# Performance work log

Hardware: AMD Instinct MI355X
Metric: run time of the kernel (lower is better)

Reference implementation:

```python
import jax, jax.numpy as jnp
import numpy as np

NUM_USERS = 100000
NUM_ITEMS = 50000
N = NUM_USERS + NUM_ITEMS
D = 64
NNZ = 4000000
BATCH = 8192
NUM_LAYERS = 3


def setup_inputs() -> dict:
    key = jax.random.key(0)
    k = jax.random.split(key, 8)
    return {
        "user_emb": jax.random.normal(k[0], (NUM_USERS, D), jnp.float32) * 0.1,
        "item_emb": jax.random.normal(k[1], (NUM_ITEMS, D), jnp.float32) * 0.1,
        # symmetric-normalized adjacency values (positive, ~1/degree scale)
        "adj_vals": jax.random.uniform(k[2], (NNZ,), jnp.float32) * (1.0 / 13.0),
        "adj_rows": jax.random.randint(k[3], (NNZ,), 0, N, jnp.int32),
        "adj_cols": jax.random.randint(k[4], (NNZ,), 0, N, jnp.int32),
        "user_idx": jax.random.randint(k[5], (BATCH,), 0, NUM_USERS, jnp.int32),
        "pos_idx": jax.random.randint(k[6], (BATCH,), 0, NUM_ITEMS, jnp.int32),
        "neg_idx": jax.random.randint(k[7], (BATCH,), 0, NUM_ITEMS, jnp.int32),
    }


def _propagate(user_emb, item_emb, adj_vals, adj_rows, adj_cols):
    # E0 = concat(user table, item table) along node axis -> [N, D]
    e = jnp.concatenate([user_emb, item_emb], axis=0)
    acc = e  # running sum over layer embeddings (E0 included)
    for _ in range(NUM_LAYERS):
        # SpMM: E <- A_norm @ E, via gather on cols + segment_sum on rows
        msg = adj_vals[:, None] * e[adj_cols]  # [NNZ, D]
        e = jax.ops.segment_sum(msg, adj_rows, num_segments=N)
        acc = acc + e
    final = acc / jnp.asarray(NUM_LAYERS + 1, e.dtype)  # mean-pool over layers
    return final


def reference(user_emb, item_emb, adj_vals, adj_rows, adj_cols,
              user_idx, pos_idx, neg_idx):
    final = _propagate(user_emb, item_emb, adj_vals, adj_rows, adj_cols)
    # split into user/item tables, then gather BPR triplets
    u = final[user_idx]                     # [B, D]
    p = final[NUM_USERS + pos_idx]          # [B, D]
    n = final[NUM_USERS + neg_idx]          # [B, D]
    pos_score = jnp.sum(u * p, axis=-1, keepdims=True)  # Dot(axes=1) -> [B,1]
    neg_score = jnp.sum(u * n, axis=-1, keepdims=True)
    return pos_score - neg_score
```

## Files before the change

### kernel.cpp

```cpp
#include <hip/hip_runtime.h>
#include <hip/hip_bf16.h>

#define D 64
#define MAXNB 1024
#define BIN_T 512
#define BIN_CHUNK 16384
#define BUCKET_BITS 9
#define BUCKET_SIZE 512
#define COL_MASK 0x3FFFF
#define ROW_SHIFT 18

static __device__ __forceinline__ float bf_lo(unsigned v) {
  return __uint_as_float(v << 16);
}
static __device__ __forceinline__ float bf_hi(unsigned v) {
  return __uint_as_float(v & 0xffff0000u);
}
static __device__ __forceinline__ unsigned pack_bf2(float a, float b) {
  __hip_bfloat16 x = __float2bfloat16(a);
  __hip_bfloat16 y = __float2bfloat16(b);
  unsigned short ux = *reinterpret_cast<unsigned short*>(&x);
  unsigned short uy = *reinterpret_cast<unsigned short*>(&y);
  return (unsigned)ux | ((unsigned)uy << 16);
}

__global__ __launch_bounds__(256) void convert_kernel(
    const float4* __restrict__ ue, const float4* __restrict__ ie,
    uint2* __restrict__ out, int nu4, int total4,
    int* __restrict__ counts, int nbp1) {
  int i = blockIdx.x * blockDim.x + threadIdx.x;
  if (i < nbp1) counts[i] = 0;
  if (i >= total4) return;
  float4 v = (i < nu4) ? ue[i] : ie[i - nu4];
  out[i] = make_uint2(pack_bf2(v.x, v.y), pack_bf2(v.z, v.w));
}

__global__ __launch_bounds__(256) void bucket_hist_kernel(
    const int* __restrict__ rows, int* __restrict__ counts, int nnz, int nb) {
  __shared__ int h[MAXNB];
  int t = threadIdx.x;
  for (int i = t; i < nb; i += 256) h[i] = 0;
  __syncthreads();
  for (int e = blockIdx.x * 256 + t; e < nnz; e += gridDim.x * 256)
    atomicAdd(&h[rows[e] >> BUCKET_BITS], 1);
  __syncthreads();
  for (int i = t; i < nb; i += 256)
    if (h[i]) atomicAdd(&counts[i], h[i]);
}

__global__ __launch_bounds__(1024) void bucket_scan_kernel(
    const int* __restrict__ counts, int* __restrict__ base,
    int* __restrict__ cursor, int nb) {
  __shared__ int lds[1024];
  int t = threadIdx.x;
  int v = (t < nb) ? counts[t] : 0;
  lds[t] = v;
  __syncthreads();
  for (int off = 1; off < 1024; off <<= 1) {
    int add = (t >= off) ? lds[t - off] : 0;
    __syncthreads();
    lds[t] += add;
    __syncthreads();
  }
  if (t < nb) {
    base[t + 1] = lds[t];
    cursor[t + 1] = lds[t];
  }
  if (t == 0) {
    base[0] = 0;
    cursor[0] = 0;
  }
}

__global__ __launch_bounds__(BIN_T) void bin_kernel(
    const float* __restrict__ vals, const int* __restrict__ rows,
    const int* __restrict__ cols, int* __restrict__ cursor,
    int2* __restrict__ binned, int nnz, int nb) {
  __shared__ int lh[MAXNB];
  int t = threadIdx.x;
  long long base_e = (long long)blockIdx.x * BIN_CHUNK;
  int end_e = (int)((base_e + BIN_CHUNK < (long long)nnz) ? base_e + BIN_CHUNK
                                                          : (long long)nnz);
  for (int i = t; i < nb; i += BIN_T) lh[i] = 0;
  __syncthreads();
  for (int e = (int)base_e + t; e < end_e; e += BIN_T)
    atomicAdd(&lh[rows[e] >> BUCKET_BITS], 1);
  __syncthreads();
  for (int i = t; i < nb; i += BIN_T) {
    int c = lh[i];
    if (c) lh[i] = atomicAdd(&cursor[i], c);
  }
  __syncthreads();
  for (int e = (int)base_e + t; e < end_e; e += BIN_T) {
    int r = rows[e];
    int pos = atomicAdd(&lh[r >> BUCKET_BITS], 1);
    binned[pos] = make_int2((cols[e] & COL_MASK) |
                                ((r & (BUCKET_SIZE - 1)) << ROW_SHIFT),
                            __float_as_int(vals[e]));
  }
}

__global__ __launch_bounds__(512) void place_kernel(
    const int2* __restrict__ binned, const int* __restrict__ base,
    int2* __restrict__ edges, int* __restrict__ row_start, int nrows, int nb) {
  __shared__ int rh[BUCKET_SIZE];
  __shared__ int cur[BUCKET_SIZE];
  int b = blockIdx.x;
  int t = threadIdx.x;
  int start = base[b];
  int end = base[b + 1];
  int r0 = b << BUCKET_BITS;
  rh[t] = 0;
  __syncthreads();
  for (int i = start + t; i < end; i += 512)
    atomicAdd(&rh[((unsigned)binned[i].x) >> ROW_SHIFT], 1);
  __syncthreads();
  int myc = rh[t];
  for (int off = 1; off < 512; off <<= 1) {
    int add = (t >= off) ? rh[t - off] : 0;
    __syncthreads();
    rh[t] += add;
    __syncthreads();
  }
  int excl = rh[t] - myc;
  int r = r0 + t;
  if (r < nrows) row_start[r] = start + excl;
  if (b == nb - 1 && t == 0) row_start[nrows] = end;
  cur[t] = start + excl;
  __syncthreads();
  for (int i = start + t; i < end; i += 512) {
    int2 rec = binned[i];
    unsigned x = (unsigned)rec.x;
    int pos = atomicAdd(&cur[x >> ROW_SHIFT], 1);
    edges[pos] = make_int2((int)(x & COL_MASK), rec.y);
  }
}

__global__ __launch_bounds__(256) void list_build_kernel(
    const int* __restrict__ ui, const int* __restrict__ pi,
    const int* __restrict__ ni, int* __restrict__ list, int batch, int nu) {
  int i = blockIdx.x * blockDim.x + threadIdx.x;
  if (i >= batch) return;
  list[3 * i] = ui[i];
  list[3 * i + 1] = nu + pi[i];
  list[3 * i + 2] = nu + ni[i];
}

__global__ __launch_bounds__(256) void spmm_bf16_kernel(
    const int* __restrict__ row_start, const int2* __restrict__ edges,
    const uint2* __restrict__ src,
    uint2* __restrict__ dst, int nrows) {
  int wid = (int)(((long long)blockIdx.x * blockDim.x + threadIdx.x) >> 6);
  if (wid >= nrows) return;
  int lane = threadIdx.x & 63;
  int sub = lane >> 4;
  int d4 = lane & 15;
  int s = row_start[wid];
  int e = row_start[wid + 1];
  float a0 = 0.f, a1 = 0.f, a2 = 0.f, a3 = 0.f;
  int j = s;
  for (; j + 16 <= e; j += 16) {
    int2 E[4];
    uint2 V[4];
    #pragma unroll
    for (int k = 0; k < 4; ++k) E[k] = edges[j + 4 * k + sub];
    #pragma unroll
    for (int k = 0; k < 4; ++k) V[k] = src[((long long)E[k].x << 4) + d4];
    #pragma unroll
    for (int k = 0; k < 4; ++k) {
      float w = __int_as_float(E[k].y);
      a0 = fmaf(w, bf_lo(V[k].x), a0);
      a1 = fmaf(w, bf_hi(V[k].x), a1);
      a2 = fmaf(w, bf_lo(V[k].y), a2);
      a3 = fmaf(w, bf_hi(V[k].y), a3);
    }
  }
  for (; j + 4 <= e; j += 4) {
    int2 ed = edges[j + sub];
    uint2 v = src[((long long)ed.x << 4) + d4];
    float w = __int_as_float(ed.y);
    a0 = fmaf(w, bf_lo(v.x), a0);
    a1 = fmaf(w, bf_hi(v.x), a1);
    a2 = fmaf(w, bf_lo(v.y), a2);
    a3 = fmaf(w, bf_hi(v.y), a3);
  }
  for (; j + 2 <= e; j += 2) {
    if ((lane & 31) < 16) {
      int2 ed = edges[j + (lane >> 5)];
      uint2 v = src[((long long)ed.x << 4) + d4];
      float w = __int_as_float(ed.y);
      a0 = fmaf(w, bf_lo(v.x), a0);
      a1 = fmaf(w, bf_hi(v.x), a1);
      a2 = fmaf(w, bf_lo(v.y), a2);
      a3 = fmaf(w, bf_hi(v.y), a3);
    }
  }
  if (j < e && sub == 0) {
    int2 ed = edges[j];
    uint2 v = src[((long long)ed.x << 4) + d4];
    float w = __int_as_float(ed.y);
    a0 = fmaf(w, bf_lo(v.x), a0);
    a1 = fmaf(w, bf_hi(v.x), a1);
    a2 = fmaf(w, bf_lo(v.y), a2);
    a3 = fmaf(w, bf_hi(v.y), a3);
  }
  a0 += __shfl_down(a0, 32, 64);
  a1 += __shfl_down(a1, 32, 64);
  a2 += __shfl_down(a2, 32, 64);
  a3 += __shfl_down(a3, 32, 64);
  a0 += __shfl_down(a0, 16, 64);
  a1 += __shfl_down(a1, 16, 64);
  a2 += __shfl_down(a2, 16, 64);
  a3 += __shfl_down(a3, 16, 64);
  if (lane < 16)
    dst[((long long)wid << 4) + d4] =
        make_uint2(pack_bf2(a0, a1), pack_bf2(a2, a3));
}

__global__ __launch_bounds__(256) void spmm_bf16_list_kernel(
    const int* __restrict__ row_start, const int2* __restrict__ edges,
    const uint2* __restrict__ src, uint2* __restrict__ dst,
    const int* __restrict__ list, int nlist) {
  int widx = (int)(((long long)blockIdx.x * blockDim.x + threadIdx.x) >> 6);
  if (widx >= nlist) return;
  int wid = list[widx];
  int lane = threadIdx.x & 63;
  int sub = lane >> 4;
  int d4 = lane & 15;
  int s = row_start[wid];
  int e = row_start[wid + 1];
  float a0 = 0.f, a1 = 0.f, a2 = 0.f, a3 = 0.f;
  int j = s;
  for (; j + 16 <= e; j += 16) {
    int2 E[4];
    uint2 V[4];
    #pragma unroll
    for (int k = 0; k < 4; ++k) E[k] = edges[j + 4 * k + sub];
    #pragma unroll
    for (int k = 0; k < 4; ++k) V[k] = src[((long long)E[k].x << 4) + d4];
    #pragma unroll
    for (int k = 0; k < 4; ++k) {
      float w = __int_as_float(E[k].y);
      a0 = fmaf(w, bf_lo(V[k].x), a0);
      a1 = fmaf(w, bf_hi(V[k].x), a1);
      a2 = fmaf(w, bf_lo(V[k].y), a2);
      a3 = fmaf(w, bf_hi(V[k].y), a3);
    }
  }
  for (; j + 4 <= e; j += 4) {
    int2 ed = edges[j + sub];
    uint2 v = src[((long long)ed.x << 4) + d4];
    float w = __int_as_float(ed.y);
    a0 = fmaf(w, bf_lo(v.x), a0);
    a1 = fmaf(w, bf_hi(v.x), a1);
    a2 = fmaf(w, bf_lo(v.y), a2);
    a3 = fmaf(w, bf_hi(v.y), a3);
  }
  for (; j + 2 <= e; j += 2) {
    if ((lane & 31) < 16) {
      int2 ed = edges[j + (lane >> 5)];
      uint2 v = src[((long long)ed.x << 4) + d4];
      float w = __int_as_float(ed.y);
      a0 = fmaf(w, bf_lo(v.x), a0);
      a1 = fmaf(w, bf_hi(v.x), a1);
      a2 = fmaf(w, bf_lo(v.y), a2);
      a3 = fmaf(w, bf_hi(v.y), a3);
    }
  }
  if (j < e && sub == 0) {
    int2 ed = edges[j];
    uint2 v = src[((long long)ed.x << 4) + d4];
    float w = __int_as_float(ed.y);
    a0 = fmaf(w, bf_lo(v.x), a0);
    a1 = fmaf(w, bf_hi(v.x), a1);
    a2 = fmaf(w, bf_lo(v.y), a2);
    a3 = fmaf(w, bf_hi(v.y), a3);
  }
  a0 += __shfl_down(a0, 32, 64);
  a1 += __shfl_down(a1, 32, 64);
  a2 += __shfl_down(a2, 32, 64);
  a3 += __shfl_down(a3, 32, 64);
  a0 += __shfl_down(a0, 16, 64);
  a1 += __shfl_down(a1, 16, 64);
  a2 += __shfl_down(a2, 16, 64);
  a3 += __shfl_down(a3, 16, 64);
  if (lane < 16)
    dst[((long long)wid << 4) + d4] =
        make_uint2(pack_bf2(a0, a1), pack_bf2(a2, a3));
}

__global__ __launch_bounds__(256) void score2_kernel(
    const float* __restrict__ ue, const float* __restrict__ ie,
    const unsigned* __restrict__ e1, const unsigned* __restrict__ e2,
    const unsigned* __restrict__ e3, const int* __restrict__ ui,
    const int* __restrict__ pi, const int* __restrict__ ni,
    float* __restrict__ out, int batch, int nu) {
  int w = (int)(((long long)blockIdx.x * blockDim.x + threadIdx.x) >> 6);
  int lane = threadIdx.x & 63;
  int half = lane >> 5;
  int d2 = lane & 31;
  int b = w * 2 + half;
  if (b >= batch) return;
  long long un = (long long)ui[b];
  int p = pi[b], n = ni[b];
  long long pn = (long long)(nu + p);
  long long nn_ = (long long)(nu + n);
  float2 U = *(const float2*)(ue + (un << 6) + (d2 << 1));
  float2 P = *(const float2*)(ie + ((long long)p << 6) + (d2 << 1));
  float2 Nv = *(const float2*)(ie + ((long long)n << 6) + (d2 << 1));
  unsigned v;
  v = e1[(un << 5) + d2]; U.x += bf_lo(v); U.y += bf_hi(v);
  v = e2[(un << 5) + d2]; U.x += bf_lo(v); U.y += bf_hi(v);
  v = e3[(un << 5) + d2]; U.x += bf_lo(v); U.y += bf_hi(v);
  v = e1[(pn << 5) + d2]; P.x += bf_lo(v); P.y += bf_hi(v);
  v = e2[(pn << 5) + d2]; P.x += bf_lo(v); P.y += bf_hi(v);
  v = e3[(pn << 5) + d2]; P.x += bf_lo(v); P.y += bf_hi(v);
  v = e1[(nn_ << 5) + d2]; Nv.x += bf_lo(v); Nv.y += bf_hi(v);
  v = e2[(nn_ << 5) + d2]; Nv.x += bf_lo(v); Nv.y += bf_hi(v);
  v = e3[(nn_ << 5) + d2]; Nv.x += bf_lo(v); Nv.y += bf_hi(v);
  float s = U.x * (P.x - Nv.x) + U.y * (P.y - Nv.y);
  #pragma unroll
  for (int off = 16; off; off >>= 1) s += __shfl_down(s, off, 32);
  if (d2 == 0) out[b] = s * (1.0f / 16.0f);
}

__global__ __launch_bounds__(256) void init_kernel(
    const float4* __restrict__ ue, const float4* __restrict__ ie,
    float4* __restrict__ e, float4* __restrict__ acc, int nu4, int total4) {
  int i = blockIdx.x * blockDim.x + threadIdx.x;
  if (i >= total4) return;
  float4 v = (i < nu4) ? ue[i] : ie[i - nu4];
  e[i] = v;
  acc[i] = v;
}

__global__ __launch_bounds__(256) void scatter_kernel(
    const float* __restrict__ vals, const int* __restrict__ rows,
    const int* __restrict__ cols, const float* __restrict__ src,
    float* __restrict__ dst, int nnz) {
  long long gid = (long long)blockIdx.x * blockDim.x + threadIdx.x;
  int e = (int)(gid >> 6);
  if (e >= nnz) return;
  int d = (int)(gid & 63);
  float w = vals[e];
  float x = src[((long long)cols[e] << 6) + d];
  atomicAdd(dst + (((long long)rows[e] << 6) + d), w * x);
}

__global__ __launch_bounds__(256) void acc_kernel(
    float4* __restrict__ acc, const float4* __restrict__ e, int total4) {
  int i = blockIdx.x * blockDim.x + threadIdx.x;
  if (i >= total4) return;
  float4 a = acc[i];
  float4 b = e[i];
  a.x += b.x; a.y += b.y; a.z += b.z; a.w += b.w;
  acc[i] = a;
}

__global__ __launch_bounds__(256) void score_kernel(
    const float* __restrict__ acc, const int* __restrict__ ui,
    const int* __restrict__ pi, const int* __restrict__ ni,
    float* __restrict__ out, int batch, int nu) {
  int wid = (int)(((long long)blockIdx.x * blockDim.x + threadIdx.x) >> 6);
  int lane = threadIdx.x & 63;
  if (wid >= batch) return;
  int u = ui[wid];
  int p = pi[wid];
  int n = ni[wid];
  float uv = acc[((long long)u << 6) + lane];
  float pv = acc[((long long)(nu + p) << 6) + lane];
  float nv = acc[((long long)(nu + n) << 6) + lane];
  float s = uv * (pv - nv);
  #pragma unroll
  for (int off = 32; off; off >>= 1) s += __shfl_down(s, off, 64);
  if (lane == 0) out[wid] = s * (1.0f / 16.0f);
}

static inline size_t align_up(size_t x) { return (x + 255) & ~(size_t)255; }

extern "C" void kernel_launch(void* const* d_in, const int* in_sizes, int n_in,
                              void* d_out, int out_size, void* d_ws, size_t ws_size,
                              hipStream_t stream) {
  const float* user_emb = (const float*)d_in[0];
  const float* item_emb = (const float*)d_in[1];
  const float* adj_vals = (const float*)d_in[2];
  const int* adj_rows = (const int*)d_in[3];
  const int* adj_cols = (const int*)d_in[4];
  const int* user_idx = (const int*)d_in[5];
  const int* pos_idx = (const int*)d_in[6];
  const int* neg_idx = (const int*)d_in[7];

  const int nnz = in_sizes[2];
  const int batch = in_sizes[5];
  const int nu = in_sizes[0] / D;
  const int ni = in_sizes[1] / D;
  const int nrows = nu + ni;
  const int nb = (nrows + BUCKET_SIZE - 1) / BUCKET_SIZE;
  const long long nd = (long long)nrows * D;
  const size_t nd_bytes = (size_t)nd * sizeof(float);
  const size_t bf_tbl = align_up((size_t)nrows * D * 2);
  const size_t edges_bytes = align_up((size_t)nnz * 8);

  const int total4 = (int)(nd / 4);
  const int nu4 = nu * D / 4;
  const int ew_blocks = (total4 + 255) / 256;

  const size_t need = 4 * bf_tbl + 2 * edges_bytes +
                      align_up((size_t)(nrows + 1) * 4) +
                      3 * align_up((size_t)(nb + 1) * 4) +
                      align_up((size_t)(3 * batch) * 4);
  const bool fast = (ws_size >= need) && (nb <= MAXNB) && (nrows <= COL_MASK);

  if (fast) {
    char* wp = (char*)d_ws;
    unsigned* e0b = (unsigned*)wp;    wp += bf_tbl;
    unsigned* e1 = (unsigned*)wp;     wp += bf_tbl;
    unsigned* e2 = (unsigned*)wp;     wp += bf_tbl;
    unsigned* e3 = (unsigned*)wp;     wp += bf_tbl;
    int2* edges = (int2*)wp;          wp += edges_bytes;
    int2* binned = (int2*)wp;         wp += edges_bytes;
    int* row_start = (int*)wp;        wp += align_up((size_t)(nrows + 1) * 4);
    int* base = (int*)wp;             wp += align_up((size_t)(nb + 1) * 4);
    int* counts = (int*)wp;           wp += align_up((size_t)(nb + 1) * 4);
    int* cursor = (int*)wp;           wp += align_up((size_t)(nb + 1) * 4);
    int* list = (int*)wp;

    convert_kernel<<<ew_blocks, 256, 0, stream>>>(
        (const float4*)user_emb, (const float4*)item_emb,
        (uint2*)e0b, nu4, total4, counts, nb + 1);

    bucket_hist_kernel<<<512, 256, 0, stream>>>(adj_rows, counts, nnz, nb);
    bucket_scan_kernel<<<1, 1024, 0, stream>>>(counts, base, cursor, nb);

    bin_kernel<<<(nnz + BIN_CHUNK - 1) / BIN_CHUNK, BIN_T, 0, stream>>>(
        adj_vals, adj_rows, adj_cols, cursor, binned, nnz, nb);
    place_kernel<<<nb, 512, 0, stream>>>(binned, base, edges, row_start,
                                         nrows, nb);

    list_build_kernel<<<(batch + 255) / 256, 256, 0, stream>>>(
        user_idx, pos_idx, neg_idx, list, batch, nu);

    const int spmm_blocks = (nrows + 3) / 4;
    spmm_bf16_kernel<<<spmm_blocks, 256, 0, stream>>>(
        row_start, edges, (const uint2*)e0b, (uint2*)e1, nrows);
    spmm_bf16_kernel<<<spmm_blocks, 256, 0, stream>>>(
        row_start, edges, (const uint2*)e1, (uint2*)e2, nrows);
    const int nlist = 3 * batch;
    spmm_bf16_list_kernel<<<(nlist + 3) / 4, 256, 0, stream>>>(
        row_start, edges, (const uint2*)e2, (uint2*)e3, list, nlist);

    score2_kernel<<<(batch / 2 + 3) / 4, 256, 0, stream>>>(
        user_emb, item_emb, e1, e2, e3, user_idx, pos_idx, neg_idx,
        (float*)d_out, batch, nu);
  } else {
    char* wp = (char*)d_ws;
    float* acc = (float*)wp;          wp += nd_bytes;
    float* e_a = (float*)wp;          wp += nd_bytes;
    float* e_b = (float*)wp;

    init_kernel<<<ew_blocks, 256, 0, stream>>>(
        (const float4*)user_emb, (const float4*)item_emb,
        (float4*)e_a, (float4*)acc, nu4, total4);
    const long long scatter_work = (long long)nnz * 64;
    const int scatter_blocks = (int)((scatter_work + 255) / 256);
    float* src = e_a;
    float* dst = e_b;
    for (int layer = 0; layer < 3; ++layer) {
      hipMemsetAsync(dst, 0, nd_bytes, stream);
      scatter_kernel<<<scatter_blocks, 256, 0, stream>>>(adj_vals, adj_rows,
                                                         adj_cols, src, dst, nnz);
      acc_kernel<<<ew_blocks, 256, 0, stream>>>((float4*)acc, (const float4*)dst,
                                                total4);
      float* t = src; src = dst; dst = t;
    }
    score_kernel<<<(batch + 3) / 4, 256, 0, stream>>>(
        acc, user_idx, pos_idx, neg_idx, (float*)d_out, batch, nu);
  }
}
```

Measured before the change: 323.8 us.

## Shrink row buckets, fuse list build, use nontemporal edge loads and 32-bit indexing

Halves the row bucket size so place_kernel runs more, smaller blocks, and guards its scan for the 256-entry histogram. The BPR list construction moves into convert_kernel, removing one launch. SpMM edge records are read as 64-bit nontemporal loads to avoid polluting cache with streaming edge data. Gather and store addresses use 32-bit unsigned math to save address instructions. The unsigned math assumes table offsets fit in 32 bits.

```diff
diff --git a/kernel.cpp b/kernel.cpp
--- a/kernel.cpp
+++ b/kernel.cpp
@@ -5,8 +5,8 @@
 #define MAXNB 1024
 #define BIN_T 512
 #define BIN_CHUNK 16384
-#define BUCKET_BITS 9
-#define BUCKET_SIZE 512
+#define BUCKET_BITS 8
+#define BUCKET_SIZE 256
 #define COL_MASK 0x3FFFF
 #define ROW_SHIFT 18
 
@@ -27,9 +27,16 @@
 __global__ __launch_bounds__(256) void convert_kernel(
     const float4* __restrict__ ue, const float4* __restrict__ ie,
     uint2* __restrict__ out, int nu4, int total4,
-    int* __restrict__ counts, int nbp1) {
+    int* __restrict__ counts, int nbp1,
+    const int* __restrict__ ui, const int* __restrict__ pi,
+    const int* __restrict__ ni, int* __restrict__ list, int batch, int nu) {
   int i = blockIdx.x * blockDim.x + threadIdx.x;
   if (i < nbp1) counts[i] = 0;
+  if (i < batch) {
+    list[3 * i] = ui[i];
+    list[3 * i + 1] = nu + pi[i];
+    list[3 * i + 2] = nu + ni[i];
+  }
   if (i >= total4) return;
   float4 v = (i < nu4) ? ue[i] : ie[i - nu4];
   out[i] = make_uint2(pack_bf2(v.x, v.y), pack_bf2(v.z, v.w));
@@ -110,23 +117,25 @@
   int start = base[b];
   int end = base[b + 1];
   int r0 = b << BUCKET_BITS;
-  rh[t] = 0;
+  if (t < BUCKET_SIZE) rh[t] = 0;
   __syncthreads();
   for (int i = start + t; i < end; i += 512)
     atomicAdd(&rh[((unsigned)binned[i].x) >> ROW_SHIFT], 1);
   __syncthreads();
-  int myc = rh[t];
-  for (int off = 1; off < 512; off <<= 1) {
-    int add = (t >= off) ? rh[t - off] : 0;
+  int myc = (t < BUCKET_SIZE) ? rh[t] : 0;
+  for (int off = 1; off < BUCKET_SIZE; off <<= 1) {
+    int add = (t >= off && t < BUCKET_SIZE) ? rh[t - off] : 0;
     __syncthreads();
-    rh[t] += add;
+    if (t < BUCKET_SIZE) rh[t] += add;
     __syncthreads();
   }
-  int excl = rh[t] - myc;
-  int r = r0 + t;
-  if (r < nrows) row_start[r] = start + excl;
-  if (b == nb - 1 && t == 0) row_start[nrows] = end;
-  cur[t] = start + excl;
+  if (t < BUCKET_SIZE) {
+    int excl = rh[t] - myc;
+    int r = r0 + t;
+    if (r < nrows) row_start[r] = start + excl;
+    if (b == nb - 1 && t == 0) row_start[nrows] = end;
+    cur[t] = start + excl;
+  }
   __syncthreads();
   for (int i = start + t; i < end; i += 512) {
     int2 rec = binned[i];
@@ -136,20 +145,11 @@
   }
 }
 
-__global__ __launch_bounds__(256) void list_build_kernel(
-    const int* __restrict__ ui, const int* __restrict__ pi,
-    const int* __restrict__ ni, int* __restrict__ list, int batch, int nu) {
-  int i = blockIdx.x * blockDim.x + threadIdx.x;
-  if (i >= batch) return;
-  list[3 * i] = ui[i];
-  list[3 * i + 1] = nu + pi[i];
-  list[3 * i + 2] = nu + ni[i];
-}
-
 __global__ __launch_bounds__(256) void spmm_bf16_kernel(
     const int* __restrict__ row_start, const int2* __restrict__ edges,
     const uint2* __restrict__ src,
     uint2* __restrict__ dst, int nrows) {
+  const long long* edges8 = (const long long*)edges;
   int wid = (int)(((long long)blockIdx.x * blockDim.x + threadIdx.x) >> 6);
   if (wid >= nrows) return;
   int lane = threadIdx.x & 63;
@@ -160,15 +160,17 @@
   float a0 = 0.f, a1 = 0.f, a2 = 0.f, a3 = 0.f;
   int j = s;
   for (; j + 16 <= e; j += 16) {
-    int2 E[4];
+    long long E[4];
     uint2 V[4];
     #pragma unroll
-    for (int k = 0; k < 4; ++k) E[k] = edges[j + 4 * k + sub];
-    #pragma unroll
-    for (int k = 0; k < 4; ++k) V[k] = src[((long long)E[k].x << 4) + d4];
+    for (int k = 0; k < 4; ++k)
+      E[k] = __builtin_nontemporal_load(edges8 + j + 4 * k + sub);
+    #pragma unroll
+    for (int k = 0; k < 4; ++k)
+      V[k] = src[((unsigned)(E[k] & COL_MASK) << 4) + (unsigned)d4];
     #pragma unroll
     for (int k = 0; k < 4; ++k) {
-      float w = __int_as_float(E[k].y);
+      float w = __int_as_float((int)(E[k] >> 32));
       a0 = fmaf(w, bf_lo(V[k].x), a0);
       a1 = fmaf(w, bf_hi(V[k].x), a1);
       a2 = fmaf(w, bf_lo(V[k].y), a2);
@@ -176,9 +178,9 @@
     }
   }
   for (; j + 4 <= e; j += 4) {
-    int2 ed = edges[j + sub];
-    uint2 v = src[((long long)ed.x << 4) + d4];
-    float w = __int_as_float(ed.y);
+    long long ed = __builtin_nontemporal_load(edges8 + j + sub);
+    uint2 v = src[((unsigned)(ed & COL_MASK) << 4) + (unsigned)d4];
+    float w = __int_as_float((int)(ed >> 32));
     a0 = fmaf(w, bf_lo(v.x), a0);
     a1 = fmaf(w, bf_hi(v.x), a1);
     a2 = fmaf(w, bf_lo(v.y), a2);
@@ -187,7 +189,7 @@
   for (; j + 2 <= e; j += 2) {
     if ((lane & 31) < 16) {
       int2 ed = edges[j + (lane >> 5)];
-      uint2 v = src[((long long)ed.x << 4) + d4];
+      uint2 v = src[((unsigned)ed.x << 4) + (unsigned)d4];
       float w = __int_as_float(ed.y);
       a0 = fmaf(w, bf_lo(v.x), a0);
       a1 = fmaf(w, bf_hi(v.x), a1);
@@ -197,7 +199,7 @@
   }
   if (j < e && sub == 0) {
     int2 ed = edges[j];
-    uint2 v = src[((long long)ed.x << 4) + d4];
+    uint2 v = src[((unsigned)ed.x << 4) + (unsigned)d4];
     float w = __int_as_float(ed.y);
     a0 = fmaf(w, bf_lo(v.x), a0);
     a1 = fmaf(w, bf_hi(v.x), a1);
@@ -213,7 +215,7 @@
   a2 += __shfl_down(a2, 16, 64);
   a3 += __shfl_down(a3, 16, 64);
   if (lane < 16)
-    dst[((long long)wid << 4) + d4] =
+    dst[((unsigned)wid << 4) + (unsigned)d4] =
         make_uint2(pack_bf2(a0, a1), pack_bf2(a2, a3));
 }
 
@@ -221,6 +223,7 @@
     const int* __restrict__ row_start, const int2* __restrict__ edges,
     const uint2* __restrict__ src, uint2* __restrict__ dst,
     const int* __restrict__ list, int nlist) {
+  const long long* edges8 = (const long long*)edges;
   int widx = (int)(((long long)blockIdx.x * blockDim.x + threadIdx.x) >> 6);
   if (widx >= nlist) return;
   int wid = list[widx];
@@ -232,15 +235,17 @@
   float a0 = 0.f, a1 = 0.f, a2 = 0.f, a3 = 0.f;
   int j = s;
   for (; j + 16 <= e; j += 16) {
-    int2 E[4];
+    long long E[4];
     uint2 V[4];
     #pragma unroll
-    for (int k = 0; k < 4; ++k) E[k] = edges[j + 4 * k + sub];
-    #pragma unroll
-    for (int k = 0; k < 4; ++k) V[k] = src[((long long)E[k].x << 4) + d4];
+    for (int k = 0; k < 4; ++k)
+      E[k] = __builtin_nontemporal_load(edges8 + j + 4 * k + sub);
+    #pragma unroll
+    for (int k = 0; k < 4; ++k)
+      V[k] = src[((unsigned)(E[k] & COL_MASK) << 4) + (unsigned)d4];
     #pragma unroll
     for (int k = 0; k < 4; ++k) {
-      float w = __int_as_float(E[k].y);
+      float w = __int_as_float((int)(E[k] >> 32));
       a0 = fmaf(w, bf_lo(V[k].x), a0);
       a1 = fmaf(w, bf_hi(V[k].x), a1);
       a2 = fmaf(w, bf_lo(V[k].y), a2);
@@ -249,7 +254,7 @@
   }
   for (; j + 4 <= e; j += 4) {
     int2 ed = edges[j + sub];
-    uint2 v = src[((long long)ed.x << 4) + d4];
+    uint2 v = src[((unsigned)ed.x << 4) + (unsigned)d4];
     float w = __int_as_float(ed.y);
     a0 = fmaf(w, bf_lo(v.x), a0);
     a1 = fmaf(w, bf_hi(v.x), a1);
@@ -259,7 +264,7 @@
   for (; j + 2 <= e; j += 2) {
     if ((lane & 31) < 16) {
       int2 ed = edges[j + (lane >> 5)];
-      uint2 v = src[((long long)ed.x << 4) + d4];
+      uint2 v = src[((unsigned)ed.x << 4) + (unsigned)d4];
       float w = __int_as_float(ed.y);
       a0 = fmaf(w, bf_lo(v.x), a0);
       a1 = fmaf(w, bf_hi(v.x), a1);
@@ -269,7 +274,7 @@
   }
   if (j < e && sub == 0) {
     int2 ed = edges[j];
-    uint2 v = src[((long long)ed.x << 4) + d4];
+    uint2 v = src[((unsigned)ed.x << 4) + (unsigned)d4];
     float w = __int_as_float(ed.y);
     a0 = fmaf(w, bf_lo(v.x), a0);
     a1 = fmaf(w, bf_hi(v.x), a1);
@@ -285,7 +290,7 @@
   a2 += __shfl_down(a2, 16, 64);
   a3 += __shfl_down(a3, 16, 64);
   if (lane < 16)
-    dst[((long long)wid << 4) + d4] =
+    dst[((unsigned)wid << 4) + (unsigned)d4] =
         make_uint2(pack_bf2(a0, a1), pack_bf2(a2, a3));
 }
 
@@ -427,7 +432,8 @@
 
     convert_kernel<<<ew_blocks, 256, 0, stream>>>(
         (const float4*)user_emb, (const float4*)item_emb,
-        (uint2*)e0b, nu4, total4, counts, nb + 1);
+        (uint2*)e0b, nu4, total4, counts, nb + 1,
+        user_idx, pos_idx, neg_idx, list, batch, nu);
 
     bucket_hist_kernel<<<512, 256, 0, stream>>>(adj_rows, counts, nnz, nb);
     bucket_scan_kernel<<<1, 1024, 0, stream>>>(counts, base, cursor, nb);
@@ -436,9 +442,6 @@
         adj_vals, adj_rows, adj_cols, cursor, binned, nnz, nb);
     place_kernel<<<nb, 512, 0, stream>>>(binned, base, edges, row_start,
                                          nrows, nb);
-
-    list_build_kernel<<<(batch + 255) / 256, 256, 0, stream>>>(
-        user_idx, pos_idx, neg_idx, list, batch, nu);
 
     const int spmm_blocks = (nrows + 3) / 4;
     spmm_bf16_kernel<<<spmm_blocks, 256, 0, stream>>>(
```

Result: slower. 353.6 us (+9.2%).
